# Optimization experiments

Hardware: AMD Instinct MI355X
Metric: run time of the kernel (lower is better)

The kernel has to match this reference:

```python
import jax, jax.numpy as jnp
import numpy as np

SIZE = (4096, 4096)   # self.size
SIGMA = 1.0           # blur_sigma
NOISE_STD = 0.01      # noise_std


def _gauss_kernel(sigma):
    # scipy.ndimage.gaussian_filter: radius = int(truncate*sigma + 0.5), truncate=4.0
    r = int(4.0 * sigma + 0.5)
    x = np.arange(-r, r + 1, dtype=np.float32)
    k = np.exp(-0.5 * (x / sigma) ** 2)
    k = k / k.sum()
    return jnp.asarray(k), r


def _blur(img, sigma):
    # img: [C, H, W]; separable Gaussian, scipy mode='reflect' == jnp symmetric pad
    k, r = _gauss_kernel(sigma)
    x = jnp.pad(img, ((0, 0), (r, r), (r, r)), mode='symmetric')
    x = x[:, None]  # [C, 1, H+2r, W+2r] (NCHW)
    kh = k.reshape(1, 1, -1, 1)
    kw = k.reshape(1, 1, 1, -1)
    x = jax.lax.conv_general_dilated(x, kh, (1, 1), 'VALID')
    x = jax.lax.conv_general_dilated(x, kw, (1, 1), 'VALID')
    return x[:, 0]  # [C, H, W]


def setup_inputs() -> dict:
    key = jax.random.key(0)
    k1, k2 = jax.random.split(key)
    img = jax.random.normal(k1, (1, 2048, 2048), dtype=jnp.float32)
    noise = jax.random.normal(k2, (1,) + SIZE, dtype=jnp.float32)
    return {"img": img, "noise": noise}


def reference(img, noise):
    # bilinear resize, align_corners=False == jax half-pixel linear resize
    img = jax.image.resize(img, (img.shape[0],) + SIZE, method='linear')
    img = jnp.flip(img, axis=2)   # horizontal flip
    img = jnp.flip(img, axis=1)   # vertical flip
    img = jnp.rot90(img, k=1, axes=(1, 2))  # rot90, k fixed to 1
    img = img + noise * NOISE_STD
    img = _blur(img, SIGMA)
    img = jnp.log1p(jnp.clip(img, 0.0))  # clamp(min=0) then log1p
    return img
```

## Files before the change

### kernel.cpp

```cpp
#include <hip/hip_runtime.h>
#include <math.h>

#define N     4096
#define NIMG  2048
#define TX    56
#define TY    32
#define DW    64
#define DH    40
#define IPR   36
#define IPP   25
#define STP   41
#define VP    65
#define S2P   57

#define KW0 0.00013383063f
#define KW1 0.00443186160f
#define KW2 0.05399112800f
#define KW3 0.24197144000f
#define KW4 0.39894346870f

__device__ __forceinline__ int symi(int g) {
    g = (g < 0) ? (-1 - g) : g;
    g = (g >= N) ? (2 * N - 1 - g) : g;
    return g;
}

__global__ __launch_bounds__(256, 7)
void TensorAugment_79216376807666_kernel(const float* __restrict__ img,
                                         const float* __restrict__ noise,
                                         float* __restrict__ out) {
    __shared__ float IP[IPR * IPP];
    __shared__ float ST[DW * STP];
    __shared__ float V[TY * VP];

    const int tid  = threadIdx.x;
    const int lane = tid & 63;
    const int wave = tid >> 6;
    const int x0 = blockIdx.x * TX;
    const int y0 = blockIdx.y * TY;

    const float kk[9] = {KW0, KW1, KW2, KW3, KW4, KW3, KW2, KW1, KW0};

    int gxa = x0 - 4, gxb = x0 + DW - 5;
    int mxa = symi(gxa), mxb = symi(gxb);
    int gxmin = min(mxa, mxb), gxmax = max(mxa, mxb);
    if (gxa <= 0) gxmin = 0;
    if (gxb >= N - 1) gxmax = N - 1;
    int umin = (N - 1) - gxmax, umax = (N - 1) - gxmin;
    int r0min = (umin - 1) >> 1;
    int r0max = (umax - 1) >> 1;
    int nrows = r0max - r0min + 2;

    int gya = y0 - 4, gyb = y0 + DH - 5;
    int mya = symi(gya), myb = symi(gyb);
    int gymin = min(mya, myb), gymax = max(mya, myb);
    if (gya <= 0) gymin = 0;
    if (gyb >= N - 1) gymax = N - 1;
    int c0min = (gymin - 1) >> 1;
    int c0max = (gymax - 1) >> 1;
    int ncols = c0max - c0min + 2;

    {
        int j  = tid & 31;
        int rr = tid >> 5;
        for (int r = rr; r < nrows; r += 8) {
            if (j < ncols) {
                int ir = min(max(r0min + r, 0), NIMG - 1);
                int ic = min(max(c0min + j, 0), NIMG - 1);
                IP[r * IPP + j] = img[ir * NIMG + ic];
            }
        }
    }
    __syncthreads();

    {
        int c   = lane;
        int gxm = symi(x0 - 4 + c);
        int u   = (N - 1) - gxm;
        int r0  = (u - 1) >> 1;
        float wr1 = (u & 1) ? 0.25f : 0.75f;
        float wr0 = 1.0f - wr1;
        int a0 = (r0 - r0min) * IPP;

#pragma unroll
        for (int k = 0; k < 10; ++k) {
            int row = wave + 4 * k;
            int gym = symi(y0 - 4 + row);
            int c0  = (gym - 1) >> 1;
            float wc1 = (gym & 1) ? 0.25f : 0.75f;
            float wc0 = 1.0f - wc1;
            int jc = c0 - c0min;

            float nv = noise[gym * N + gxm];
            float f0 = IP[a0 + jc],       f1 = IP[a0 + jc + 1];
            float f2 = IP[a0 + IPP + jc], f3 = IP[a0 + IPP + jc + 1];
            float top = fmaf(wc0, f0, wc1 * f1);
            float bot = fmaf(wc0, f2, wc1 * f3);
            float d = fmaf(wr0, top, wr1 * bot) + 0.01f * nv;
            ST[c * STP + row] = d;
        }
    }
    __syncthreads();

    {
        int c = lane;
        int rbase = wave * 8;
        float win[16];
        int ab = c * STP + rbase;
#pragma unroll
        for (int k = 0; k < 16; ++k) win[k] = ST[ab + k];
#pragma unroll
        for (int j = 0; j < 8; ++j) {
            float acc = 0.0f;
#pragma unroll
            for (int i = 0; i < 9; ++i) acc = fmaf(kk[i], win[j + i], acc);
            V[(rbase + j) * VP + c] = acc;
        }
    }
    __syncthreads();

    {
        int r = tid >> 3;
        int s = tid & 7;
        float w2[15];
        int vb = r * VP + s * 7;
#pragma unroll
        for (int k = 0; k < 15; ++k) w2[k] = V[vb + k];
#pragma unroll
        for (int j = 0; j < 7; ++j) {
            float acc = 0.0f;
#pragma unroll
            for (int i = 0; i < 9; ++i) acc = fmaf(kk[i], w2[j + i], acc);
            acc = fmaxf(acc, 0.0f);
            ST[r * S2P + s * 7 + j] = __logf(1.0f + acc);
        }
    }
    __syncthreads();

    for (int r = wave; r < TY; r += 4) {
        int gx = x0 + lane;
        if (lane < TX && gx < N)
            out[(y0 + r) * N + gx] = ST[r * S2P + lane];
    }
}

extern "C" void kernel_launch(void* const* d_in, const int* in_sizes, int n_in,
                              void* d_out, int out_size, void* d_ws, size_t ws_size,
                              hipStream_t stream) {
    const float* img   = (const float*)d_in[0];
    const float* noise = (const float*)d_in[1];
    float* out = (float*)d_out;

    dim3 grid((N + TX - 1) / TX, N / TY);
    TensorAugment_79216376807666_kernel<<<grid, 256, 0, stream>>>(img, noise, out);
}
```

Before: 148.9 us.

## Enlarge tile to 56x56, add interior fast path with vectorized noise and output

Tiles grow from 56x32 to 56x56, which cuts the vertical halo overhead, and the input-patch and vertical-blur buffers now share one LDS region. Interior blocks take a specialized resample path: each thread reads a float4 of noise and computes four upsampled columns from shared bilinear taps. The final horizontal pass writes float2 stores straight to global memory, dropping the staging round-trip and one barrier. The costs are more LDS and registers per block (launch bounds 7 to 5), idle threads in the last pass (only 224 of 256 work), and divergent edge handling.

```diff
diff --git a/kernel.cpp b/kernel.cpp
--- a/kernel.cpp
+++ b/kernel.cpp
@@ -4,14 +4,12 @@
 #define N     4096
 #define NIMG  2048
 #define TX    56
-#define TY    32
+#define TY    56
 #define DW    64
-#define DH    40
-#define IPR   36
-#define IPP   25
-#define STP   41
+#define DH    64
+#define IPP   35
+#define STP   65
 #define VP    65
-#define S2P   57
 
 #define KW0 0.00013383063f
 #define KW1 0.00443186160f
@@ -25,19 +23,22 @@
     return g;
 }
 
-__global__ __launch_bounds__(256, 7)
+__global__ __launch_bounds__(256, 5)
 void TensorAugment_79216376807666_kernel(const float* __restrict__ img,
                                          const float* __restrict__ noise,
                                          float* __restrict__ out) {
-    __shared__ float IP[IPR * IPP];
     __shared__ float ST[DW * STP];
-    __shared__ float V[TY * VP];
+    __shared__ float UN[TY * VP];
+    float* const IP = UN;
+    float* const V  = UN;
 
     const int tid  = threadIdx.x;
     const int lane = tid & 63;
     const int wave = tid >> 6;
-    const int x0 = blockIdx.x * TX;
-    const int y0 = blockIdx.y * TY;
+    const int bx = blockIdx.x, by = blockIdx.y;
+    const int x0 = bx * TX;
+    const int y0 = by * TY;
+    const bool interior = (bx >= 1) && (bx <= 72) && (by >= 1) && (by <= 72);
 
     const float kk[9] = {KW0, KW1, KW2, KW3, KW4, KW3, KW2, KW1, KW0};
 
@@ -61,19 +62,47 @@
     int ncols = c0max - c0min + 2;
 
     {
-        int j  = tid & 31;
-        int rr = tid >> 5;
-        for (int r = rr; r < nrows; r += 8) {
-            if (j < ncols) {
-                int ir = min(max(r0min + r, 0), NIMG - 1);
-                int ic = min(max(c0min + j, 0), NIMG - 1);
-                IP[r * IPP + j] = img[ir * NIMG + ic];
+        int c = tid & 31;
+        for (int r = tid >> 5; r < nrows; r += 8) {
+            int ir = min(max(r0min + r, 0), NIMG - 1);
+            int ic = min(max(c0min + c, 0), NIMG - 1);
+            IP[r * IPP + c] = img[ir * NIMG + ic];
+            if (c < ncols - 32) {
+                int ic2 = min(max(c0min + 32 + c, 0), NIMG - 1);
+                IP[r * IPP + 32 + c] = img[ir * NIMG + ic2];
             }
         }
     }
     __syncthreads();
 
-    {
+    if (interior) {
+        int g  = lane & 15;
+        int rr = lane >> 4;
+        int sbase = (30 - 2 * g) * IPP;
+        const float* npz = noise + (size_t)(y0 - 4) * N + (x0 - 4) + 4 * g;
+#pragma unroll
+        for (int it = 0; it < 4; ++it) {
+            int row = it * 16 + wave * 4 + rr;
+            int jc  = (row + 1) >> 1;
+            float wc1 = (row & 1) ? 0.25f : 0.75f;
+            float wc0 = 1.0f - wc1;
+            float4 nv = *reinterpret_cast<const float4*>(npz + (size_t)row * N);
+            int b = sbase + jc;
+            float t0 = fmaf(wc0, IP[b],           wc1 * IP[b + 1]);
+            float t1 = fmaf(wc0, IP[b + IPP],     wc1 * IP[b + IPP + 1]);
+            float t2 = fmaf(wc0, IP[b + 2 * IPP], wc1 * IP[b + 2 * IPP + 1]);
+            float t3 = fmaf(wc0, IP[b + 3 * IPP], wc1 * IP[b + 3 * IPP + 1]);
+            float D0 = fmaf(0.75f, t2, 0.25f * t3);
+            float D1 = fmaf(0.25f, t1, 0.75f * t2);
+            float D2 = fmaf(0.75f, t1, 0.25f * t2);
+            float D3 = fmaf(0.25f, t0, 0.75f * t1);
+            int sb = (4 * g) * STP + row;
+            ST[sb]           = fmaf(0.01f, nv.x, D0);
+            ST[sb + STP]     = fmaf(0.01f, nv.y, D1);
+            ST[sb + 2 * STP] = fmaf(0.01f, nv.z, D2);
+            ST[sb + 3 * STP] = fmaf(0.01f, nv.w, D3);
+        }
+    } else {
         int c   = lane;
         int gxm = symi(x0 - 4 + c);
         int u   = (N - 1) - gxm;
@@ -81,66 +110,74 @@
         float wr1 = (u & 1) ? 0.25f : 0.75f;
         float wr0 = 1.0f - wr1;
         int a0 = (r0 - r0min) * IPP;
-
 #pragma unroll
-        for (int k = 0; k < 10; ++k) {
+        for (int k = 0; k < 16; ++k) {
             int row = wave + 4 * k;
             int gym = symi(y0 - 4 + row);
             int c0  = (gym - 1) >> 1;
             float wc1 = (gym & 1) ? 0.25f : 0.75f;
             float wc0 = 1.0f - wc1;
             int jc = c0 - c0min;
-
-            float nv = noise[gym * N + gxm];
+            float nv = noise[(size_t)gym * N + gxm];
             float f0 = IP[a0 + jc],       f1 = IP[a0 + jc + 1];
             float f2 = IP[a0 + IPP + jc], f3 = IP[a0 + IPP + jc + 1];
             float top = fmaf(wc0, f0, wc1 * f1);
             float bot = fmaf(wc0, f2, wc1 * f3);
-            float d = fmaf(wr0, top, wr1 * bot) + 0.01f * nv;
-            ST[c * STP + row] = d;
+            ST[c * STP + row] = fmaf(wr0, top, wr1 * bot) + 0.01f * nv;
         }
     }
     __syncthreads();
 
     {
-        int c = lane;
-        int rbase = wave * 8;
-        float win[16];
-        int ab = c * STP + rbase;
+        int c  = lane;
+        int rb = wave * 14;
+        float win[22];
+        int ab = c * STP + rb;
 #pragma unroll
-        for (int k = 0; k < 16; ++k) win[k] = ST[ab + k];
+        for (int k = 0; k < 22; ++k) win[k] = ST[ab + k];
 #pragma unroll
-        for (int j = 0; j < 8; ++j) {
+        for (int j = 0; j < 14; ++j) {
             float acc = 0.0f;
 #pragma unroll
             for (int i = 0; i < 9; ++i) acc = fmaf(kk[i], win[j + i], acc);
-            V[(rbase + j) * VP + c] = acc;
+            V[(rb + j) * VP + c] = acc;
         }
     }
     __syncthreads();
 
     {
-        int r = tid >> 3;
-        int s = tid & 7;
-        float w2[15];
-        int vb = r * VP + s * 7;
+        int r = tid >> 2;
+        int s = tid & 3;
+        if (r < TY) {
+            float w2[22];
+            int vb = r * VP + s * 14;
 #pragma unroll
-        for (int k = 0; k < 15; ++k) w2[k] = V[vb + k];
+            for (int k = 0; k < 22; ++k) w2[k] = V[vb + k];
+            float res[14];
 #pragma unroll
-        for (int j = 0; j < 7; ++j) {
-            float acc = 0.0f;
+            for (int j = 0; j < 14; ++j) {
+                float acc = 0.0f;
 #pragma unroll
-            for (int i = 0; i < 9; ++i) acc = fmaf(kk[i], w2[j + i], acc);
-            acc = fmaxf(acc, 0.0f);
-            ST[r * S2P + s * 7 + j] = __logf(1.0f + acc);
+                for (int i = 0; i < 9; ++i) acc = fmaf(kk[i], w2[j + i], acc);
+                acc = fmaxf(acc, 0.0f);
+                res[j] = __logf(1.0f + acc);
+            }
+            if (interior) {
+                float2* op = reinterpret_cast<float2*>(out + (size_t)(y0 + r) * N + x0 + s * 14);
+#pragma unroll
+                for (int j2 = 0; j2 < 7; ++j2)
+                    op[j2] = make_float2(res[2 * j2], res[2 * j2 + 1]);
+            } else {
+                int gy = y0 + r;
+                if (gy < N) {
+#pragma unroll
+                    for (int j = 0; j < 14; ++j) {
+                        int gx = x0 + s * 14 + j;
+                        if (gx < N) out[(size_t)gy * N + gx] = res[j];
+                    }
+                }
+            }
         }
-    }
-    __syncthreads();
-
-    for (int r = wave; r < TY; r += 4) {
-        int gx = x0 + lane;
-        if (lane < TX && gx < N)
-            out[(y0 + r) * N + gx] = ST[r * S2P + lane];
     }
 }
 
@@ -151,6 +188,6 @@
     const float* noise = (const float*)d_in[1];
     float* out = (float*)d_out;
 
-    dim3 grid((N + TX - 1) / TX, N / TY);
+    dim3 grid((N + TX - 1) / TX, (N + TY - 1) / TY);
     TensorAugment_79216376807666_kernel<<<grid, 256, 0, stream>>>(img, noise, out);
 }
```

New measurement: 160.8 us. 1.08x slower.

## Add interior fast path with vectorized noise loads and alias shared buffers

Applied to the files above, without the earlier changes.

Interior tiles, which need no reflect padding, take a specialized path. There each lane loads four consecutive noise values as a float4 and computes four bilinear outputs from shared rows, replacing the per-element symmetric index math and scalar loads. The IP and V shared buffers now share one allocation, and launch bounds rise from 7 to 8 blocks per CU to raise occupancy. This adds branch divergence between border and interior blocks and relies on hardcoded interior bounds and lane mapping.

```diff
diff --git a/kernel.cpp b/kernel.cpp
--- a/kernel.cpp
+++ b/kernel.cpp
@@ -25,19 +25,22 @@
     return g;
 }
 
-__global__ __launch_bounds__(256, 7)
+__global__ __launch_bounds__(256, 8)
 void TensorAugment_79216376807666_kernel(const float* __restrict__ img,
                                          const float* __restrict__ noise,
                                          float* __restrict__ out) {
-    __shared__ float IP[IPR * IPP];
     __shared__ float ST[DW * STP];
-    __shared__ float V[TY * VP];
+    __shared__ float UN[TY * VP];
+    float* const IP = UN;
+    float* const V  = UN;
 
     const int tid  = threadIdx.x;
     const int lane = tid & 63;
     const int wave = tid >> 6;
-    const int x0 = blockIdx.x * TX;
-    const int y0 = blockIdx.y * TY;
+    const int bx = blockIdx.x, by = blockIdx.y;
+    const int x0 = bx * TX;
+    const int y0 = by * TY;
+    const bool interior = (bx >= 1) && (bx <= 72) && (by >= 1) && (by <= 126);
 
     const float kk[9] = {KW0, KW1, KW2, KW3, KW4, KW3, KW2, KW1, KW0};
 
@@ -61,19 +64,47 @@
     int ncols = c0max - c0min + 2;
 
     {
-        int j  = tid & 31;
-        int rr = tid >> 5;
-        for (int r = rr; r < nrows; r += 8) {
-            if (j < ncols) {
+        int c = tid & 31;
+        for (int r = tid >> 5; r < nrows; r += 8) {
+            if (c < ncols) {
                 int ir = min(max(r0min + r, 0), NIMG - 1);
-                int ic = min(max(c0min + j, 0), NIMG - 1);
-                IP[r * IPP + j] = img[ir * NIMG + ic];
+                int ic = min(max(c0min + c, 0), NIMG - 1);
+                IP[r * IPP + c] = img[ir * NIMG + ic];
             }
         }
     }
     __syncthreads();
 
-    {
+    if (interior) {
+        int g  = lane & 15;
+        int rr = lane >> 4;
+        int sbase = (30 - 2 * g) * IPP;
+        const float* npz = noise + (size_t)(y0 - 4) * N + (x0 - 4) + 4 * g;
+#pragma unroll
+        for (int it = 0; it < 3; ++it) {
+            int row = it * 16 + wave * 4 + rr;
+            if (row < DH) {
+                int jc  = (row + 1) >> 1;
+                float wc1 = (row & 1) ? 0.25f : 0.75f;
+                float wc0 = 1.0f - wc1;
+                float4 nv = *reinterpret_cast<const float4*>(npz + (size_t)row * N);
+                int b = sbase + jc;
+                float t0 = fmaf(wc0, IP[b],           wc1 * IP[b + 1]);
+                float t1 = fmaf(wc0, IP[b + IPP],     wc1 * IP[b + IPP + 1]);
+                float t2 = fmaf(wc0, IP[b + 2 * IPP], wc1 * IP[b + 2 * IPP + 1]);
+                float t3 = fmaf(wc0, IP[b + 3 * IPP], wc1 * IP[b + 3 * IPP + 1]);
+                float D0 = fmaf(0.75f, t2, 0.25f * t3);
+                float D1 = fmaf(0.25f, t1, 0.75f * t2);
+                float D2 = fmaf(0.75f, t1, 0.25f * t2);
+                float D3 = fmaf(0.25f, t0, 0.75f * t1);
+                int sb = (4 * g) * STP + row;
+                ST[sb]           = fmaf(0.01f, nv.x, D0);
+                ST[sb + STP]     = fmaf(0.01f, nv.y, D1);
+                ST[sb + 2 * STP] = fmaf(0.01f, nv.z, D2);
+                ST[sb + 3 * STP] = fmaf(0.01f, nv.w, D3);
+            }
+        }
+    } else {
         int c   = lane;
         int gxm = symi(x0 - 4 + c);
         int u   = (N - 1) - gxm;
@@ -81,7 +112,6 @@
         float wr1 = (u & 1) ? 0.25f : 0.75f;
         float wr0 = 1.0f - wr1;
         int a0 = (r0 - r0min) * IPP;
-
 #pragma unroll
         for (int k = 0; k < 10; ++k) {
             int row = wave + 4 * k;
@@ -90,23 +120,21 @@
             float wc1 = (gym & 1) ? 0.25f : 0.75f;
             float wc0 = 1.0f - wc1;
             int jc = c0 - c0min;
-
             float nv = noise[gym * N + gxm];
             float f0 = IP[a0 + jc],       f1 = IP[a0 + jc + 1];
             float f2 = IP[a0 + IPP + jc], f3 = IP[a0 + IPP + jc + 1];
             float top = fmaf(wc0, f0, wc1 * f1);
             float bot = fmaf(wc0, f2, wc1 * f3);
-            float d = fmaf(wr0, top, wr1 * bot) + 0.01f * nv;
-            ST[c * STP + row] = d;
+            ST[c * STP + row] = fmaf(wr0, top, wr1 * bot) + 0.01f * nv;
         }
     }
     __syncthreads();
 
     {
-        int c = lane;
-        int rbase = wave * 8;
+        int c  = lane;
+        int rb = wave * 8;
         float win[16];
-        int ab = c * STP + rbase;
+        int ab = c * STP + rb;
 #pragma unroll
         for (int k = 0; k < 16; ++k) win[k] = ST[ab + k];
 #pragma unroll
@@ -114,7 +142,7 @@
             float acc = 0.0f;
 #pragma unroll
             for (int i = 0; i < 9; ++i) acc = fmaf(kk[i], win[j + i], acc);
-            V[(rbase + j) * VP + c] = acc;
+            V[(rb + j) * VP + c] = acc;
         }
     }
     __syncthreads();
@@ -140,7 +168,7 @@
     for (int r = wave; r < TY; r += 4) {
         int gx = x0 + lane;
         if (lane < TX && gx < N)
-            out[(y0 + r) * N + gx] = ST[r * S2P + lane];
+            out[(size_t)(y0 + r) * N + gx] = ST[r * S2P + lane];
     }
 }
 
```

New measurement: 144.5 us. 3.0% less time.
